# Kernel optimization log

Hardware: AMD Instinct MI355X
Metric: run time of the kernel (lower is better)

## Reference

```python
import jax, jax.numpy as jnp
import numpy as np

B, H, S, D = 16, 12, 1024, 64  # batch, heads, seq, head_dim (dim=768, num_head=12)


def setup_inputs() -> dict:
    key = jax.random.key(0)
    ks = jax.random.split(key, 9)
    sc = 1.0 / np.sqrt(D)
    return {
        "x": jax.random.normal(ks[0], (B, H, S, D), dtype=jnp.float32),
        "Wq": jax.random.normal(ks[1], (D, D), dtype=jnp.float32) * sc,
        "bq": jax.random.normal(ks[2], (D,), dtype=jnp.float32) * 0.02,
        "Wk": jax.random.normal(ks[3], (D, D), dtype=jnp.float32) * sc,
        "bk": jax.random.normal(ks[4], (D,), dtype=jnp.float32) * 0.02,
        "Wv": jax.random.normal(ks[5], (D, D), dtype=jnp.float32) * sc,
        "bv": jax.random.normal(ks[6], (D,), dtype=jnp.float32) * 0.02,
        "Wo": jax.random.normal(ks[7], (D, D), dtype=jnp.float32) * sc,
        "bo": jax.random.normal(ks[8], (D,), dtype=jnp.float32) * 0.02,
    }


def reference(x, Wq, bq, Wk, bk, Wv, bv, Wo, bo):
    # torch Linear: y = x @ W^T + b, applied to last dim (head_dim)
    q = jnp.einsum("bhsd,ed->bhse", x, Wq) + bq
    k = jnp.einsum("bhsd,ed->bhse", x, Wk) + bk
    v = jnp.einsum("bhsd,ed->bhse", x, Wv) + bv
    scores = jnp.einsum("bhqd,bhkd->bhqk", q, k) / jnp.sqrt(jnp.float32(q.shape[-1]))
    attn = jax.nn.softmax(scores, axis=-1)
    out = jnp.einsum("bhqk,bhkd->bhqd", attn, v)
    out = jnp.einsum("bhsd,ed->bhse", out, Wo) + bo
    return out
```

## Files before the change

### kernel.cpp

```cpp
#include <hip/hip_runtime.h>
#include <math.h>


typedef __bf16 bf16x8 __attribute__((ext_vector_type(8)));
typedef float  f32x4  __attribute__((ext_vector_type(4)));

#define MFMA(a, b, c) __builtin_amdgcn_mfma_f32_16x16x32_bf16((a), (b), (c), 0, 0, 0)

static constexpr int S = 1024;
static constexpr int PAD = 72;
static constexpr size_t NE = 196608ull * 64ull;
static constexpr float QSCALE = 0.125f * 1.4426950408889634f;

__device__ inline unsigned long long pack4bf(float a, float b, float c, float d) {
    union { __bf16 h[4]; unsigned long long u; } pk;
    pk.h[0] = (__bf16)a; pk.h[1] = (__bf16)b; pk.h[2] = (__bf16)c; pk.h[3] = (__bf16)d;
    return pk.u;
}

union frag_u { bf16x8 v; unsigned long long u[2]; };

__global__ void prep(const float* __restrict__ x,
                     const float* __restrict__ Wq, const float* __restrict__ Wk,
                     const float* __restrict__ Wv, const float* __restrict__ Wo,
                     __bf16* __restrict__ xb,
                     __bf16* __restrict__ wqb, __bf16* __restrict__ wkb,
                     __bf16* __restrict__ wvb, __bf16* __restrict__ wob)
{
    const int bid = blockIdx.x;
    if (bid < 6144) {
        size_t p = ((size_t)bid * 256 + threadIdx.x) * 8;
        float4 a = *(const float4*)(x + p);
        float4 b = *(const float4*)(x + p + 4);
        union { unsigned long long u64[2]; uint4 v; } pk;
        pk.u64[0] = pack4bf(a.x, a.y, a.z, a.w);
        pk.u64[1] = pack4bf(b.x, b.y, b.z, b.w);
        *(uint4*)(xb + p) = pk.v;
    } else {
        const int wb  = bid - 6144;
        const int grp = wb >> 2;
        const int p   = (((wb & 3) * 256) + threadIdx.x) * 4;
        if (grp == 3) {
            int e = p >> 6, s = p & 63;
            int h = s >> 5, qp = (s >> 3) & 3, tb = (s >> 2) & 1;
            int d0 = 32 * h + 16 * tb + 4 * qp;
            float4 v = *(const float4*)(Wo + e * 64 + d0);
            *(unsigned long long*)(wob + p) = pack4bf(v.x, v.y, v.z, v.w);
        } else {
            const float* src = (grp == 0) ? Wq : (grp == 1) ? Wk : Wv;
            __bf16*      dst = (grp == 0) ? wqb : (grp == 1) ? wkb : wvb;
            float4 v = *(const float4*)(src + p);
            *(unsigned long long*)(dst + p) = pack4bf(v.x, v.y, v.z, v.w);
        }
    }
}

__global__ __launch_bounds__(256, 2) void attn(
    const __bf16* __restrict__ xb,
    const __bf16* __restrict__ wqb, const __bf16* __restrict__ wkb,
    const __bf16* __restrict__ wvb, const __bf16* __restrict__ wob,
    const float* __restrict__ bq, const float* __restrict__ bk,
    const float* __restrict__ bv, const float* __restrict__ bo,
    float* __restrict__ out)
{
    __shared__ __align__(16) union {
        __bf16 xq[256][PAD];
        struct {
            __bf16 k[64][PAD];
            __bf16 v[64][PAD];
        } m;
    } L;
    __shared__ __align__(16) __bf16 lw[2][8][64][8];

    const int tid = threadIdx.x;
    const int w = tid >> 6, lane = tid & 63, m = lane & 15, quad = lane >> 4;
    const int bh = blockIdx.x;
    const int q0 = blockIdx.y * 256 + w * 64;

    const __bf16* xqbase = xb + ((size_t)bh * 1024 + blockIdx.y * 256) * 64;
    #pragma unroll
    for (int i = tid * 8, it = 0; it < 8; i += 2048, it++) {
        int r = i >> 6, c = i & 63;
        *(uint4*)&L.xq[r][c] = *(const uint4*)(xqbase + i);
    }
    #pragma unroll
    for (int c = tid; c < 1024; c += 256) {
        int mtx = c >> 9, rest = c & 511;
        int fe = rest >> 6, ln = rest & 63;
        int mm = ln & 15, qq = ln >> 4;
        int et = fe >> 1, half = fe & 1;
        const __bf16* src = (mtx ? wvb : wkb) + (size_t)(et * 16 + mm) * 64 + half * 32 + qq * 8;
        *(uint4*)&lw[mtx][fe][ln][0] = *(const uint4*)src;
    }
    __syncthreads();

    bf16x8 xqf[4][2];
    #pragma unroll
    for (int g = 0; g < 4; g++) {
        xqf[g][0] = *(const bf16x8*)&L.xq[w * 64 + g * 16 + m][quad * 8];
        xqf[g][1] = *(const bf16x8*)&L.xq[w * 64 + g * 16 + m][32 + quad * 8];
    }
    #pragma unroll
    for (int et = 0; et < 4; et++) {
        bf16x8 wf0 = *(const bf16x8*)(wqb + (size_t)(et * 16 + m) * 64 + quad * 8);
        bf16x8 wf1 = *(const bf16x8*)(wqb + (size_t)(et * 16 + m) * 64 + 32 + quad * 8);
        float4 bias = *(const float4*)(bq + et * 16 + quad * 4);
        #pragma unroll
        for (int g = 0; g < 4; g++) {
            f32x4 acc = {0.f, 0.f, 0.f, 0.f};
            acc = MFMA(wf0, xqf[g][0], acc);
            acc = MFMA(wf1, xqf[g][1], acc);
            *(unsigned long long*)&L.xq[w * 64 + g * 16 + m][et * 16 + quad * 4] =
                pack4bf((acc[0] + bias.x) * QSCALE, (acc[1] + bias.y) * QSCALE,
                        (acc[2] + bias.z) * QSCALE, (acc[3] + bias.w) * QSCALE);
        }
    }
    bf16x8 qf[4][2];
    #pragma unroll
    for (int g = 0; g < 4; g++) {
        qf[g][0] = *(const bf16x8*)&L.xq[w * 64 + g * 16 + m][quad * 8];
        qf[g][1] = *(const bf16x8*)&L.xq[w * 64 + g * 16 + m][32 + quad * 8];
    }
    __syncthreads();

    float4 bkr[4];
    float  bvr[4];
    #pragma unroll
    for (int et = 0; et < 4; et++) {
        bkr[et] = *(const float4*)(bk + et * 16 + quad * 4);
        bvr[et] = bv[et * 16 + m];
    }

    f32x4 o[4][4];
    float lsum[4] = {0.f, 0.f, 0.f, 0.f};
    #pragma unroll
    for (int g = 0; g < 4; g++)
        #pragma unroll
        for (int n = 0; n < 4; n++) o[g][n] = {0.f, 0.f, 0.f, 0.f};

    const __bf16* xkey = xb + (size_t)bh * 1024 * 64;
    const int p0 = 32 * (w >> 1) + 8 * quad + 4 * (w & 1);

    bf16x8 xk0 = *(const bf16x8*)(xkey + (size_t)(w * 16 + m) * 64 + quad * 8);
    bf16x8 xk1 = *(const bf16x8*)(xkey + (size_t)(w * 16 + m) * 64 + 32 + quad * 8);

    for (int kb = 0; kb < 16; kb++) {
        __syncthreads();

        bf16x8 nx0, nx1;
        if (kb < 15) {
            const __bf16* xrow = xkey + (size_t)((kb + 1) * 64 + w * 16 + m) * 64;
            nx0 = *(const bf16x8*)(xrow + quad * 8);
            nx1 = *(const bf16x8*)(xrow + 32 + quad * 8);
        }

        #pragma unroll
        for (int et = 0; et < 4; et++) {
            bf16x8 kw0 = *(const bf16x8*)&lw[0][et * 2 + 0][lane][0];
            bf16x8 kw1 = *(const bf16x8*)&lw[0][et * 2 + 1][lane][0];
            f32x4 ka = {0.f, 0.f, 0.f, 0.f};
            ka = MFMA(kw0, xk0, ka);
            ka = MFMA(kw1, xk1, ka);
            *(unsigned long long*)&L.m.k[w * 16 + m][et * 16 + quad * 4] =
                pack4bf(ka[0] + bkr[et].x, ka[1] + bkr[et].y,
                        ka[2] + bkr[et].z, ka[3] + bkr[et].w);
            bf16x8 vw0 = *(const bf16x8*)&lw[1][et * 2 + 0][lane][0];
            bf16x8 vw1 = *(const bf16x8*)&lw[1][et * 2 + 1][lane][0];
            f32x4 va = {0.f, 0.f, 0.f, 0.f};
            va = MFMA(xk0, vw0, va);
            va = MFMA(xk1, vw1, va);
            *(unsigned long long*)&L.m.v[et * 16 + m][p0] =
                pack4bf(va[0] + bvr[et], va[1] + bvr[et],
                        va[2] + bvr[et], va[3] + bvr[et]);
        }
        __syncthreads();

        __builtin_amdgcn_s_setprio(1);
        #pragma unroll
        for (int gp = 0; gp < 2; gp++) {
            frag_u pb[2][2];
            #pragma unroll
            for (int t = 0; t < 4; t++) {
                bf16x8 ka0 = *(const bf16x8*)&L.m.k[t * 16 + m][quad * 8];
                bf16x8 ka1 = *(const bf16x8*)&L.m.k[t * 16 + m][32 + quad * 8];
                #pragma unroll
                for (int gl = 0; gl < 2; gl++) {
                    const int g = gp * 2 + gl;
                    f32x4 acc = {0.f, 0.f, 0.f, 0.f};
                    acc = MFMA(ka0, qf[g][0], acc);
                    acc = MFMA(ka1, qf[g][1], acc);
                    float e0 = __builtin_amdgcn_exp2f(acc[0]);
                    float e1 = __builtin_amdgcn_exp2f(acc[1]);
                    float e2 = __builtin_amdgcn_exp2f(acc[2]);
                    float e3 = __builtin_amdgcn_exp2f(acc[3]);
                    lsum[g] += (e0 + e1) + (e2 + e3);
                    pb[gl][t >> 1].u[t & 1] = pack4bf(e0, e1, e2, e3);
                }
            }
            #pragma unroll
            for (int n = 0; n < 4; n++) {
                bf16x8 va0 = *(const bf16x8*)&L.m.v[n * 16 + m][quad * 8];
                bf16x8 va1 = *(const bf16x8*)&L.m.v[n * 16 + m][32 + quad * 8];
                #pragma unroll
                for (int gl = 0; gl < 2; gl++) {
                    const int g = gp * 2 + gl;
                    o[g][n] = MFMA(va0, pb[gl][0].v, o[g][n]);
                    o[g][n] = MFMA(va1, pb[gl][1].v, o[g][n]);
                }
            }
        }
        __builtin_amdgcn_s_setprio(0);

        xk0 = nx0; xk1 = nx1;
    }

    #pragma unroll
    for (int g = 0; g < 4; g++) {
        lsum[g] += __shfl_xor(lsum[g], 16);
        lsum[g] += __shfl_xor(lsum[g], 32);
    }

    bf16x8 wf[4][2];
    #pragma unroll
    for (int et = 0; et < 4; et++) {
        wf[et][0] = *(const bf16x8*)(wob + (size_t)(et * 16 + m) * 64 + quad * 8);
        wf[et][1] = *(const bf16x8*)(wob + (size_t)(et * 16 + m) * 64 + 32 + quad * 8);
    }
    float biasr[4];
    #pragma unroll
    for (int et = 0; et < 4; et++) biasr[et] = bo[et * 16 + m];

    #pragma unroll
    for (int g = 0; g < 4; g++) {
        const float inv = 1.f / lsum[g];
        frag_u af0, af1;
        af0.u[0] = pack4bf(o[g][0][0] * inv, o[g][0][1] * inv, o[g][0][2] * inv, o[g][0][3] * inv);
        af0.u[1] = pack4bf(o[g][1][0] * inv, o[g][1][1] * inv, o[g][1][2] * inv, o[g][1][3] * inv);
        af1.u[0] = pack4bf(o[g][2][0] * inv, o[g][2][1] * inv, o[g][2][2] * inv, o[g][2][3] * inv);
        af1.u[1] = pack4bf(o[g][3][0] * inv, o[g][3][1] * inv, o[g][3][2] * inv, o[g][3][3] * inv);
        #pragma unroll
        for (int et = 0; et < 4; et++) {
            f32x4 acc = {0.f, 0.f, 0.f, 0.f};
            acc = MFMA(af0.v, wf[et][0], acc);
            acc = MFMA(af1.v, wf[et][1], acc);
            #pragma unroll
            for (int r = 0; r < 4; r++) {
                size_t row = (size_t)bh * S + q0 + g * 16 + quad * 4 + r;
                out[row * 64 + et * 16 + m] = acc[r] + biasr[et];
            }
        }
    }
}

extern "C" void kernel_launch(void* const* d_in, const int* in_sizes, int n_in,
                              void* d_out, int out_size, void* d_ws, size_t ws_size,
                              hipStream_t stream) {
    const float* x  = (const float*)d_in[0];
    const float* Wq = (const float*)d_in[1];
    const float* bq = (const float*)d_in[2];
    const float* Wk = (const float*)d_in[3];
    const float* bk = (const float*)d_in[4];
    const float* Wv = (const float*)d_in[5];
    const float* bv = (const float*)d_in[6];
    const float* Wo = (const float*)d_in[7];
    const float* bo = (const float*)d_in[8];
    float* out = (float*)d_out;

    __bf16* xb  = (__bf16*)d_ws;
    __bf16* wob = xb + NE;
    __bf16* wqb = wob + 4096;
    __bf16* wkb = wqb + 4096;
    __bf16* wvb = wkb + 4096;

    prep<<<6160, 256, 0, stream>>>(x, Wq, Wk, Wv, Wo, xb, wqb, wkb, wvb, wob);
    attn<<<dim3(192, 4), 256, 0, stream>>>(xb, wqb, wkb, wvb, wob,
                                           bq, bk, bv, bo, out);
}
```

Baseline: 195.3 us.

## Double-buffer K/V tiles in LDS to cut one barrier per block

K and V projection tiles in shared memory become double-buffered. The next block's K/V are computed into the alternate buffer right after the current block's attention math, so each iteration needs one barrier instead of two. This removes a sync point and lets projection work overlap with other waves' attention. In exchange, K/V LDS use doubles (still inside the xq union) and register pressure rises somewhat.

```diff
diff --git a/kernel.cpp b/kernel.cpp
--- a/kernel.cpp
+++ b/kernel.cpp
@@ -66,8 +66,8 @@
     __shared__ __align__(16) union {
         __bf16 xq[256][PAD];
         struct {
-            __bf16 k[64][PAD];
-            __bf16 v[64][PAD];
+            __bf16 k[2][64][PAD];
+            __bf16 v[2][64][PAD];
         } m;
     } L;
     __shared__ __align__(16) __bf16 lw[2][8][64][8];
@@ -141,19 +141,9 @@
     const __bf16* xkey = xb + (size_t)bh * 1024 * 64;
     const int p0 = 32 * (w >> 1) + 8 * quad + 4 * (w & 1);
 
-    bf16x8 xk0 = *(const bf16x8*)(xkey + (size_t)(w * 16 + m) * 64 + quad * 8);
-    bf16x8 xk1 = *(const bf16x8*)(xkey + (size_t)(w * 16 + m) * 64 + 32 + quad * 8);
-
-    for (int kb = 0; kb < 16; kb++) {
-        __syncthreads();
-
-        bf16x8 nx0, nx1;
-        if (kb < 15) {
-            const __bf16* xrow = xkey + (size_t)((kb + 1) * 64 + w * 16 + m) * 64;
-            nx0 = *(const bf16x8*)(xrow + quad * 8);
-            nx1 = *(const bf16x8*)(xrow + 32 + quad * 8);
-        }
-
+    {
+        bf16x8 xk0 = *(const bf16x8*)(xkey + (size_t)(w * 16 + m) * 64 + quad * 8);
+        bf16x8 xk1 = *(const bf16x8*)(xkey + (size_t)(w * 16 + m) * 64 + 32 + quad * 8);
         #pragma unroll
         for (int et = 0; et < 4; et++) {
             bf16x8 kw0 = *(const bf16x8*)&lw[0][et * 2 + 0][lane][0];
@@ -161,7 +151,7 @@
             f32x4 ka = {0.f, 0.f, 0.f, 0.f};
             ka = MFMA(kw0, xk0, ka);
             ka = MFMA(kw1, xk1, ka);
-            *(unsigned long long*)&L.m.k[w * 16 + m][et * 16 + quad * 4] =
+            *(unsigned long long*)&L.m.k[0][w * 16 + m][et * 16 + quad * 4] =
                 pack4bf(ka[0] + bkr[et].x, ka[1] + bkr[et].y,
                         ka[2] + bkr[et].z, ka[3] + bkr[et].w);
             bf16x8 vw0 = *(const bf16x8*)&lw[1][et * 2 + 0][lane][0];
@@ -169,11 +159,22 @@
             f32x4 va = {0.f, 0.f, 0.f, 0.f};
             va = MFMA(xk0, vw0, va);
             va = MFMA(xk1, vw1, va);
-            *(unsigned long long*)&L.m.v[et * 16 + m][p0] =
+            *(unsigned long long*)&L.m.v[0][et * 16 + m][p0] =
                 pack4bf(va[0] + bvr[et], va[1] + bvr[et],
                         va[2] + bvr[et], va[3] + bvr[et]);
         }
+    }
+
+    for (int kb = 0; kb < 16; kb++) {
         __syncthreads();
+        const int cur = kb & 1;
+
+        bf16x8 nx0, nx1;
+        if (kb < 15) {
+            const __bf16* xrow = xkey + (size_t)((kb + 1) * 64 + w * 16 + m) * 64;
+            nx0 = *(const bf16x8*)(xrow + quad * 8);
+            nx1 = *(const bf16x8*)(xrow + 32 + quad * 8);
+        }
 
         __builtin_amdgcn_s_setprio(1);
         #pragma unroll
@@ -181,8 +182,8 @@
             frag_u pb[2][2];
             #pragma unroll
             for (int t = 0; t < 4; t++) {
-                bf16x8 ka0 = *(const bf16x8*)&L.m.k[t * 16 + m][quad * 8];
-                bf16x8 ka1 = *(const bf16x8*)&L.m.k[t * 16 + m][32 + quad * 8];
+                bf16x8 ka0 = *(const bf16x8*)&L.m.k[cur][t * 16 + m][quad * 8];
+                bf16x8 ka1 = *(const bf16x8*)&L.m.k[cur][t * 16 + m][32 + quad * 8];
                 #pragma unroll
                 for (int gl = 0; gl < 2; gl++) {
                     const int g = gp * 2 + gl;
@@ -199,8 +200,8 @@
             }
             #pragma unroll
             for (int n = 0; n < 4; n++) {
-                bf16x8 va0 = *(const bf16x8*)&L.m.v[n * 16 + m][quad * 8];
-                bf16x8 va1 = *(const bf16x8*)&L.m.v[n * 16 + m][32 + quad * 8];
+                bf16x8 va0 = *(const bf16x8*)&L.m.v[cur][n * 16 + m][quad * 8];
+                bf16x8 va1 = *(const bf16x8*)&L.m.v[cur][n * 16 + m][32 + quad * 8];
                 #pragma unroll
                 for (int gl = 0; gl < 2; gl++) {
                     const int g = gp * 2 + gl;
@@ -211,7 +212,27 @@
         }
         __builtin_amdgcn_s_setprio(0);
 
-        xk0 = nx0; xk1 = nx1;
+        if (kb < 15) {
+            #pragma unroll
+            for (int et = 0; et < 4; et++) {
+                bf16x8 kw0 = *(const bf16x8*)&lw[0][et * 2 + 0][lane][0];
+                bf16x8 kw1 = *(const bf16x8*)&lw[0][et * 2 + 1][lane][0];
+                f32x4 ka = {0.f, 0.f, 0.f, 0.f};
+                ka = MFMA(kw0, nx0, ka);
+                ka = MFMA(kw1, nx1, ka);
+                *(unsigned long long*)&L.m.k[cur ^ 1][w * 16 + m][et * 16 + quad * 4] =
+                    pack4bf(ka[0] + bkr[et].x, ka[1] + bkr[et].y,
+                            ka[2] + bkr[et].z, ka[3] + bkr[et].w);
+                bf16x8 vw0 = *(const bf16x8*)&lw[1][et * 2 + 0][lane][0];
+                bf16x8 vw1 = *(const bf16x8*)&lw[1][et * 2 + 1][lane][0];
+                f32x4 va = {0.f, 0.f, 0.f, 0.f};
+                va = MFMA(nx0, vw0, va);
+                va = MFMA(nx1, vw1, va);
+                *(unsigned long long*)&L.m.v[cur ^ 1][et * 16 + m][p0] =
+                    pack4bf(va[0] + bvr[et], va[1] + bvr[et],
+                            va[2] + bvr[et], va[3] + bvr[et]);
+            }
+        }
     }
 
     #pragma unroll
```

New measurement: 202.4 us. 1.04x slower.
